# Kernel tuning notes

Measured on AMD Instinct MI355X. Metric: run time of the kernel, lower is better.

## Reference

```python
import jax, jax.numpy as jnp
import numpy as np

THRESH = 0.05
VAR0, VAR1 = 0.1, 0.2


def _scale(cls, reg, stride):
    # cls: (1,2,H,W)  reg: (1,4,H,W)
    p = jax.nn.softmax(cls, axis=1)
    score_map = p[0, 1]                      # (H, W)
    H, W = score_map.shape
    mask = score_map > THRESH                # torch.where(ocls[:,1] > 0.05) positions
    # Faithful to the source's indexing bug: poss[0] is the batch index (always 0
    # since B=1) used as hindex, poss[1] is the H index used as windex. So every
    # thresholded position (h, w) decodes values that depend only on h, with
    # hindex=0 and windex=h. Requires H == W (square maps), which holds here.
    h = jnp.arange(H, dtype=cls.dtype)
    s = jnp.asarray(stride, dtype=cls.dtype)
    axc = s / 2 + h * s                      # stride/2 + windex*stride, windex=h
    s4 = s * 4
    loc = reg[0, :, 0, :]                    # (4, W): reg[0, :, hindex=0, windex=h]
    # decode: cx = axc + loc0*var0*s4 ; w = s4*exp(loc2*var1) ; x1 = cx - w/2
    cx = axc + loc[0] * VAR0 * s4
    x1 = cx - (s4 * jnp.exp(loc[2] * VAR1)) / 2  # source sets x1=y1=x2=y2=box[0][0]
    sc = p[0, 1, 0, :]                       # score at (hindex=0, windex=h)
    row = jnp.stack([x1, x1, x1, x1, sc], axis=-1)   # (H, 5)
    rows = jnp.broadcast_to(row[:, None, :], (H, W, 5))
    # dense masked output (fixed shape for jit); non-thresholded rows are zero
    return jnp.where(mask[:, :, None], rows, jnp.zeros((), cls.dtype)).reshape(H * W, 5)


def setup_inputs() -> dict:
    key = jax.random.key(0)
    sizes = [2048, 1024, 512, 256, 128, 64]
    inp = {}
    for i, hw in enumerate(sizes):
        k1, k2, key = jax.random.split(key, 3)
        inp[f"cls{i}"] = jax.random.normal(k1, (1, 2, hw, hw), dtype=jnp.float32)
        inp[f"reg{i}"] = jax.random.normal(k2, (1, 4, hw, hw), dtype=jnp.float32)
    return inp


def reference(cls0, reg0, cls1, reg1, cls2, reg2, cls3, reg3, cls4, reg4, cls5, reg5):
    pairs = [(cls0, reg0), (cls1, reg1), (cls2, reg2),
             (cls3, reg3), (cls4, reg4), (cls5, reg5)]
    outs = [_scale(c, r, 2 ** (i + 2)) for i, (c, r) in enumerate(pairs)]
    return jnp.concatenate(outs, axis=0)     # (sum H_i*W_i, 5)
```

## Files before the change

kernel.cpp:

```cpp
#include <hip/hip_runtime.h>


namespace {

constexpr float LN19 = 2.9444389791664403f;

struct Params {
  const float* cls[6];
  const float* reg[6];
  float2* ws;
  float* out;
  unsigned rowBase[6];
  unsigned outBase[6];
  unsigned blockBase[6];
  unsigned logW[6];
};

template <typename T>
__device__ __forceinline__ T sel6(const T (&a)[6], int lvl) {
  T r = a[0];
#pragma unroll
  for (int L = 1; L < 6; ++L) r = (lvl == L) ? a[L] : r;
  return r;
}

}

__global__ __launch_bounds__(256) void pp_rows(Params p) {
  unsigned gid = blockIdx.x * 256u + threadIdx.x;
  if (gid >= 4032u) return;
  int lvl = 0;
#pragma unroll
  for (int L = 1; L < 6; ++L) lvl += (gid >= p.rowBase[L]) ? 1 : 0;
  unsigned i    = gid - sel6(p.rowBase, lvl);
  unsigned logW = sel6(p.logW, lvl);
  unsigned HW   = 1u << (2u * logW);
  const float* cls = sel6(p.cls, lvl);
  const float* reg = sel6(p.reg, lvl);

  float s  = (float)(4 << lvl);
  float s4 = 4.0f * s;
  float c0 = cls[i];
  float c1 = cls[HW + i];
  float sc = 1.0f / (1.0f + expf(c0 - c1));
  float l0 = reg[i];
  float l2 = reg[2u * HW + i];
  float axc = 0.5f * s + (float)i * s;
  float cx  = axc + (l0 * 0.1f) * s4;
  float x1  = cx - (s4 * expf(l2 * 0.2f)) * 0.5f;
  p.ws[gid] = make_float2(x1, sc);
}

__global__ __launch_bounds__(256) void pp_out(Params p) {
  unsigned b = blockIdx.x;
  int lvl = 0;
#pragma unroll
  for (int L = 1; L < 6; ++L) lvl += (b >= p.blockBase[L]) ? 1 : 0;
  unsigned bl   = b - sel6(p.blockBase, lvl);
  unsigned logW = sel6(p.logW, lvl);
  unsigned HW   = 1u << (2u * logW);
  const float*  cls = sel6(p.cls, lvl);
  const float2* ws  = p.ws + sel6(p.rowBase, lvl);
  float*        out = p.out + sel6(p.outBase, lvl);

  unsigned f  = (bl * 256u + threadIdx.x) * 4u;
  unsigned r0 = f / 5u;
  unsigned k0 = f - r0 * 5u;
  unsigned r1 = r0 + 1u;
  if (r1 > HW - 1u) r1 = HW - 1u;

  float d0 = cls[r0] - cls[HW + r0];
  float d1 = cls[r1] - cls[HW + r1];
  float2 w0 = ws[r0 >> logW];
  float2 w1 = ws[r1 >> logW];
  float a0 = (d0 < LN19) ? w0.x : 0.0f;
  float b0 = (d0 < LN19) ? w0.y : 0.0f;
  float a1 = (d1 < LN19) ? w1.x : 0.0f;
  float b1 = (d1 < LN19) ? w1.y : 0.0f;

  float v[4];
  unsigned k = k0;
  bool sec = false;
#pragma unroll
  for (int u = 0; u < 4; ++u) {
    float va = sec ? a1 : a0;
    float vb = sec ? b1 : b0;
    v[u] = (k == 4u) ? vb : va;
    ++k;
    if (k == 5u) { k = 0u; sec = true; }
  }
  *reinterpret_cast<float4*>(out + f) = make_float4(v[0], v[1], v[2], v[3]);
}

extern "C" void kernel_launch(void* const* d_in, const int* in_sizes, int n_in,
                              void* d_out, int out_size, void* d_ws, size_t ws_size,
                              hipStream_t stream) {
  Params p;
  unsigned rowBase = 0, outBase = 0, blockBase = 0;
  for (int l = 0; l < 6; ++l) {
    unsigned logW = 11u - (unsigned)l;
    unsigned W = 1u << logW;
    p.cls[l] = (const float*)d_in[2 * l];
    p.reg[l] = (const float*)d_in[2 * l + 1];
    p.logW[l] = logW;
    p.rowBase[l] = rowBase;
    p.outBase[l] = outBase;
    p.blockBase[l] = blockBase;
    rowBase  += W;
    outBase  += W * W * 5u;
    blockBase += (W * W * 5u) >> 10;
  }
  p.ws  = (float2*)d_ws;
  p.out = (float*)d_out;

  pp_rows<<<16, 256, 0, stream>>>(p);
  pp_out<<<blockBase, 256, 0, stream>>>(p);
}
```

Baseline: 220.5 us.

## Fuse per-row decode into output kernel and use nontemporal stores

Drops the separate row-decode kernel and its workspace round trip. Each thread of the output kernel now recomputes the softmax score and box decode for its one or two rows straight from cls/reg, which removes a launch and a dependency between kernels. The output store becomes a nontemporal vector store so the large write stream bypasses cache. In exchange, every thread repeats the exp computations and the gathered loads, which should mostly hit in cache because many threads share a row.

```diff
diff --git a/kernel.cpp b/kernel.cpp
--- a/kernel.cpp
+++ b/kernel.cpp
@@ -5,12 +5,12 @@
 
 constexpr float LN19 = 2.9444389791664403f;
 
+typedef float floatx4 __attribute__((ext_vector_type(4)));
+
 struct Params {
   const float* cls[6];
   const float* reg[6];
-  float2* ws;
   float* out;
-  unsigned rowBase[6];
   unsigned outBase[6];
   unsigned blockBase[6];
   unsigned logW[6];
@@ -26,32 +26,7 @@
 
 }
 
-__global__ __launch_bounds__(256) void pp_rows(Params p) {
-  unsigned gid = blockIdx.x * 256u + threadIdx.x;
-  if (gid >= 4032u) return;
-  int lvl = 0;
-#pragma unroll
-  for (int L = 1; L < 6; ++L) lvl += (gid >= p.rowBase[L]) ? 1 : 0;
-  unsigned i    = gid - sel6(p.rowBase, lvl);
-  unsigned logW = sel6(p.logW, lvl);
-  unsigned HW   = 1u << (2u * logW);
-  const float* cls = sel6(p.cls, lvl);
-  const float* reg = sel6(p.reg, lvl);
-
-  float s  = (float)(4 << lvl);
-  float s4 = 4.0f * s;
-  float c0 = cls[i];
-  float c1 = cls[HW + i];
-  float sc = 1.0f / (1.0f + expf(c0 - c1));
-  float l0 = reg[i];
-  float l2 = reg[2u * HW + i];
-  float axc = 0.5f * s + (float)i * s;
-  float cx  = axc + (l0 * 0.1f) * s4;
-  float x1  = cx - (s4 * expf(l2 * 0.2f)) * 0.5f;
-  p.ws[gid] = make_float2(x1, sc);
-}
-
-__global__ __launch_bounds__(256) void pp_out(Params p) {
+__global__ __launch_bounds__(256) void pp_fused(Params p) {
   unsigned b = blockIdx.x;
   int lvl = 0;
 #pragma unroll
@@ -59,9 +34,9 @@
   unsigned bl   = b - sel6(p.blockBase, lvl);
   unsigned logW = sel6(p.logW, lvl);
   unsigned HW   = 1u << (2u * logW);
-  const float*  cls = sel6(p.cls, lvl);
-  const float2* ws  = p.ws + sel6(p.rowBase, lvl);
-  float*        out = p.out + sel6(p.outBase, lvl);
+  const float* cls = sel6(p.cls, lvl);
+  const float* reg = sel6(p.reg, lvl);
+  float*       out = p.out + sel6(p.outBase, lvl);
 
   unsigned f  = (bl * 256u + threadIdx.x) * 4u;
   unsigned r0 = f / 5u;
@@ -71,14 +46,41 @@
 
   float d0 = cls[r0] - cls[HW + r0];
   float d1 = cls[r1] - cls[HW + r1];
-  float2 w0 = ws[r0 >> logW];
-  float2 w1 = ws[r1 >> logW];
-  float a0 = (d0 < LN19) ? w0.x : 0.0f;
-  float b0 = (d0 < LN19) ? w0.y : 0.0f;
-  float a1 = (d1 < LN19) ? w1.x : 0.0f;
-  float b1 = (d1 < LN19) ? w1.y : 0.0f;
 
-  float v[4];
+  unsigned i0 = r0 >> logW;
+  unsigned i1 = r1 >> logW;
+  float s  = (float)(4 << lvl);
+  float s4 = 4.0f * s;
+
+  float sc0, x10;
+  {
+    float c0 = cls[i0];
+    float c1 = cls[HW + i0];
+    sc0 = 1.0f / (1.0f + expf(c0 - c1));
+    float l0 = reg[i0];
+    float l2 = reg[2u * HW + i0];
+    float axc = 0.5f * s + (float)i0 * s;
+    float cx  = axc + (l0 * 0.1f) * s4;
+    x10 = cx - (s4 * expf(l2 * 0.2f)) * 0.5f;
+  }
+  float sc1 = sc0, x11 = x10;
+  if (i1 != i0) {
+    float c0 = cls[i1];
+    float c1 = cls[HW + i1];
+    sc1 = 1.0f / (1.0f + expf(c0 - c1));
+    float l0 = reg[i1];
+    float l2 = reg[2u * HW + i1];
+    float axc = 0.5f * s + (float)i1 * s;
+    float cx  = axc + (l0 * 0.1f) * s4;
+    x11 = cx - (s4 * expf(l2 * 0.2f)) * 0.5f;
+  }
+
+  float a0 = (d0 < LN19) ? x10 : 0.0f;
+  float b0 = (d0 < LN19) ? sc0 : 0.0f;
+  float a1 = (d1 < LN19) ? x11 : 0.0f;
+  float b1 = (d1 < LN19) ? sc1 : 0.0f;
+
+  floatx4 v;
   unsigned k = k0;
   bool sec = false;
 #pragma unroll
@@ -89,30 +91,26 @@
     ++k;
     if (k == 5u) { k = 0u; sec = true; }
   }
-  *reinterpret_cast<float4*>(out + f) = make_float4(v[0], v[1], v[2], v[3]);
+  __builtin_nontemporal_store(v, reinterpret_cast<floatx4*>(out + f));
 }
 
 extern "C" void kernel_launch(void* const* d_in, const int* in_sizes, int n_in,
                               void* d_out, int out_size, void* d_ws, size_t ws_size,
                               hipStream_t stream) {
   Params p;
-  unsigned rowBase = 0, outBase = 0, blockBase = 0;
+  unsigned outBase = 0, blockBase = 0;
   for (int l = 0; l < 6; ++l) {
     unsigned logW = 11u - (unsigned)l;
     unsigned W = 1u << logW;
     p.cls[l] = (const float*)d_in[2 * l];
     p.reg[l] = (const float*)d_in[2 * l + 1];
     p.logW[l] = logW;
-    p.rowBase[l] = rowBase;
     p.outBase[l] = outBase;
     p.blockBase[l] = blockBase;
-    rowBase  += W;
     outBase  += W * W * 5u;
     blockBase += (W * W * 5u) >> 10;
   }
-  p.ws  = (float2*)d_ws;
   p.out = (float*)d_out;
 
-  pp_rows<<<16, 256, 0, stream>>>(p);
-  pp_out<<<blockBase, 256, 0, stream>>>(p);
+  pp_fused<<<blockBase, 256, 0, stream>>>(p);
 }
```

After: 216.2 us. 1.02x faster.
